# Kernel optimization log

Measured on AMD Instinct MI355X. Metric: run time of the kernel, lower is better.

## Reference

```python
import jax, jax.numpy as jnp
import numpy as np

K = 20  # kNN neighbours (conf.k)

def knn_edge_feats(x, k):
    """x: [B, C, N] -> edge features [B, 2C, N, k] (central || neighbor-central)."""
    xt = jnp.swapaxes(x, 1, 2)                       # [B, N, C]
    sq = jnp.sum(xt * xt, axis=2, keepdims=True)     # [B, N, 1]
    dist = -2.0 * jnp.einsum('bnc,bcm->bnm', xt, x) + sq + jnp.swapaxes(sq, 1, 2)  # [B,N,N]
    idx = jnp.argsort(dist, axis=2)[:, :, 1:k + 1]   # [B, N, k], skip self (col 0)
    nbrs = jax.vmap(lambda xb, ib: xb[:, ib])(x, idx)  # [B, C, N, k]
    central = x[:, :, :, None]                        # [B, C, N, 1]
    return jnp.concatenate([jnp.broadcast_to(central, nbrs.shape), nbrs - central], axis=1)

def edge_conv(x, w, b, k):
    """1x1 conv over edge features, max over k.  x:[B,C,N], w:[Fout,2C], b:[Fout]."""
    ee = knn_edge_feats(x, k)                                   # [B, 2C, N, k]
    y = jnp.einsum('oc,bcnk->bonk', w, ee) + b[None, :, None, None]
    return jnp.max(y, axis=3)                                   # [B, Fout, N]

def setup_inputs() -> dict:
    key = jax.random.key(0)
    ks = iter(jax.random.split(key, 32))
    B, N = 16, 2048
    d = {}
    d['x'] = jax.random.normal(next(ks), (B, 3, N), dtype=jnp.float32)
    def w(shape, scale):
        return jax.random.normal(next(ks), shape, dtype=jnp.float32) * scale
    d['ec0_w'] = w((64, 6), 0.3);    d['ec0_b'] = w((64,), 0.05)
    d['ec1_w'] = w((64, 128), 0.08); d['ec1_b'] = w((64,), 0.05)
    d['ec2_w'] = w((64, 128), 0.08); d['ec2_b'] = w((64,), 0.05)
    d['ec3_w'] = w((128, 128), 0.08); d['ec3_b'] = w((128,), 0.05)
    d['conv0_w'] = w((1024, 320), 0.05); d['conv0_b'] = w((1024,), 0.05)
    d['conv0_s'] = jax.random.uniform(next(ks), (1024,), minval=0.5, maxval=1.5)
    d['conv0_t'] = w((1024,), 0.05)
    d['fc0_w'] = w((512, 1024), 0.03); d['fc0_b'] = w((512,), 0.05)
    d['fc0_s'] = jax.random.uniform(next(ks), (512,), minval=0.5, maxval=1.5)
    d['fc0_t'] = w((512,), 0.05)
    d['fc1_w'] = w((256, 512), 0.04); d['fc1_b'] = w((256,), 0.05)
    d['fc1_s'] = jax.random.uniform(next(ks), (256,), minval=0.5, maxval=1.5)
    d['fc1_t'] = w((256,), 0.05)
    d['fc2_w'] = w((40, 256), 0.06); d['fc2_b'] = w((40,), 0.05)
    d['fc2_s'] = jax.random.uniform(next(ks), (40,), minval=0.5, maxval=1.5)
    d['fc2_t'] = w((40,), 0.05)
    return d

def reference(x, ec0_w, ec0_b, ec1_w, ec1_b, ec2_w, ec2_b, ec3_w, ec3_b,
              conv0_w, conv0_b, conv0_s, conv0_t,
              fc0_w, fc0_b, fc0_s, fc0_t,
              fc1_w, fc1_b, fc1_s, fc1_t,
              fc2_w, fc2_b, fc2_s, fc2_t):
    x1 = edge_conv(x, ec0_w, ec0_b, K)    # [B, 64, N]
    x2 = edge_conv(x1, ec1_w, ec1_b, K)   # [B, 64, N]
    x3 = edge_conv(x2, ec2_w, ec2_b, K)   # [B, 64, N]
    x4 = edge_conv(x3, ec3_w, ec3_b, K)   # [B, 128, N]
    h = jnp.concatenate([x1, x2, x3, x4], axis=1)              # [B, 320, N]
    # conv1dbr: 1x1 conv + BN(affine folded into s,t) + ReLU
    h = jnp.einsum('oc,bcn->bon', conv0_w, h) + conv0_b[None, :, None]
    h = jax.nn.relu(h * conv0_s[None, :, None] + conv0_t[None, :, None])  # [B, 1024, N]
    g = jnp.max(h, axis=2)                                     # [B, 1024]
    # fcbr blocks: linear + BN + ReLU
    g = jax.nn.relu((g @ fc0_w.T + fc0_b) * fc0_s + fc0_t)     # [B, 512]
    g = jax.nn.relu((g @ fc1_w.T + fc1_b) * fc1_s + fc1_t)     # [B, 256]
    g = jax.nn.relu((g @ fc2_w.T + fc2_b) * fc2_s + fc2_t)     # [B, 40]
    return g
```

## Files before the change

kernel.cpp:

```cpp
#include <hip/hip_runtime.h>

#define DEVINL __device__ __forceinline__

static const int NPTS = 2048;

typedef __attribute__((ext_vector_type(8))) short bf16x8;
typedef __attribute__((ext_vector_type(4))) float f32x4;

DEVINL unsigned fenc(float x) {
    int b = __float_as_int(x);
    return (b < 0) ? ~(unsigned)b : ((unsigned)b | 0x80000000u);
}
DEVINL float fdec(unsigned u) {
    return (u & 0x80000000u) ? __int_as_float((int)(u & 0x7fffffffu))
                             : __int_as_float((int)~u);
}
DEVINL unsigned long long u64min(unsigned long long a, unsigned long long b) {
    return (b < a) ? b : a;
}
DEVINL unsigned short f2bf(float x) {
    unsigned u = __float_as_uint(x);
    return (unsigned short)((u + 0x7fffu + ((u >> 16) & 1u)) >> 16);
}
DEVINL float bf2f(unsigned short h) { return __uint_as_float(((unsigned)h) << 16); }

DEVINL void topk20(float v[32], unsigned long long* cand, int lane,
                   int* __restrict__ Iout, int outBase) {
    float t16[16];
#pragma unroll
    for (int i = 0; i < 16; ++i) t16[i] = fminf(v[i], v[i + 16]);
#pragma unroll
    for (int i = 0; i < 8; ++i) t16[i] = fminf(t16[i], t16[i + 8]);
#pragma unroll
    for (int i = 0; i < 4; ++i) t16[i] = fminf(t16[i], t16[i + 4]);
    float s = fminf(fminf(t16[0], t16[1]), fminf(t16[2], t16[3]));
#pragma unroll
    for (int k = 2; k <= 64; k <<= 1) {
#pragma unroll
        for (int j = k >> 1; j >= 1; j >>= 1) {
            float o = __shfl_xor(s, j);
            bool keepmin = (((lane & j) == 0) == ((lane & k) == 0));
            s = keepmin ? fminf(s, o) : fmaxf(s, o);
        }
    }
    const float tau = __shfl(s, 19);
    int cnt = 0;
#pragma unroll
    for (int j = 0; j < 32; ++j) {
        bool pass = (v[j] <= tau);
        unsigned long long mask = __ballot(pass);
        if (pass) {
            int pos = cnt + (int)__popcll(mask & ((1ull << lane) - 1ull));
            if (pos < 64) {
                int col = lane * 4 + (j & 3) + ((j >> 2) << 8);
                cand[pos] = ((unsigned long long)fenc(v[j]) << 32) | (unsigned)col;
            }
        }
        cnt += (int)__popcll(mask);
    }
    if (cnt <= 64) {
        unsigned long long key = (lane < cnt) ? cand[lane] : ~0ull;
#pragma unroll
        for (int k = 2; k <= 64; k <<= 1) {
#pragma unroll
            for (int j = k >> 1; j >= 1; j >>= 1) {
                unsigned long long o = __shfl_xor(key, j);
                bool keepmin = (((lane & j) == 0) == ((lane & k) == 0));
                unsigned long long mn = u64min(key, o);
                unsigned long long mx = (key ^ o) ^ mn;
                key = keepmin ? mn : mx;
            }
        }
        if (lane < 20) Iout[outBase + lane] = (int)(unsigned)(key & 0xffffffffu);
    } else {
        unsigned long long vk[32];
#pragma unroll
        for (int j = 0; j < 32; ++j) {
            int col = lane * 4 + (j & 3) + ((j >> 2) << 8);
            vk[j] = ((unsigned long long)fenc(v[j]) << 32) | (unsigned)col;
        }
        unsigned long long last = 0ull;
        for (int it = 0; it < 20; ++it) {
            unsigned long long q16[16];
#pragma unroll
            for (int i = 0; i < 16; ++i) {
                unsigned long long a = (vk[i] > last) ? vk[i] : ~0ull;
                unsigned long long c = (vk[i + 16] > last) ? vk[i + 16] : ~0ull;
                q16[i] = u64min(a, c);
            }
#pragma unroll
            for (int i = 0; i < 8; ++i) q16[i] = u64min(q16[i], q16[i + 8]);
#pragma unroll
            for (int i = 0; i < 4; ++i) q16[i] = u64min(q16[i], q16[i + 4]);
            unsigned long long best = u64min(u64min(q16[0], q16[1]), u64min(q16[2], q16[3]));
#pragma unroll
            for (int off = 32; off >= 1; off >>= 1) {
                unsigned long long o = __shfl_down(best, off);
                best = u64min(best, o);
            }
            best = __shfl(best, 0);
            if (lane == 0) Iout[outBase + it] = (int)(unsigned)(best & 0xffffffffu);
            last = best;
        }
    }
}

__global__ __launch_bounds__(256) void knnfused_kernel(const float* __restrict__ X, int bs,
                                                       int* __restrict__ Iout) {
    extern __shared__ char smem[];
    float* Dr = (float*)smem;
    float* As = (float*)(smem + 65536);
    unsigned long long* cand = (unsigned long long*)(smem + 67584);
    const int N = NPTS, K = 20;
    const int b = blockIdx.y, n0 = blockIdx.x * 8;
    const float* __restrict__ Xb = X + (size_t)b * bs;
    const int tid = threadIdx.x;
    if (tid < 128) {
        int c = tid >> 1, r4 = (tid & 1) * 4;
        *(float4*)&As[c * 8 + r4] = *(const float4*)&Xb[(size_t)c * N + n0 + r4];
    }
    __syncthreads();
    const int m0 = tid * 4, m1 = 1024 + tid * 4;
    float acc0[8][4], acc1[8][4], sq0[4], sq1[4];
#pragma unroll
    for (int r = 0; r < 8; ++r)
#pragma unroll
        for (int j = 0; j < 4; ++j) { acc0[r][j] = 0.f; acc1[r][j] = 0.f; }
#pragma unroll
    for (int j = 0; j < 4; ++j) { sq0[j] = 0.f; sq1[j] = 0.f; }
#pragma unroll 4
    for (int c = 0; c < 64; ++c) {
        float4 b0 = *(const float4*)&Xb[(size_t)c * N + m0];
        float4 b1 = *(const float4*)&Xb[(size_t)c * N + m1];
        float4 a0 = *(const float4*)&As[c * 8];
        float4 a1 = *(const float4*)&As[c * 8 + 4];
        sq0[0] += b0.x * b0.x; sq0[1] += b0.y * b0.y;
        sq0[2] += b0.z * b0.z; sq0[3] += b0.w * b0.w;
        sq1[0] += b1.x * b1.x; sq1[1] += b1.y * b1.y;
        sq1[2] += b1.z * b1.z; sq1[3] += b1.w * b1.w;
        float av[8] = {a0.x, a0.y, a0.z, a0.w, a1.x, a1.y, a1.z, a1.w};
#pragma unroll
        for (int r = 0; r < 8; ++r) {
            acc0[r][0] += av[r] * b0.x; acc0[r][1] += av[r] * b0.y;
            acc0[r][2] += av[r] * b0.z; acc0[r][3] += av[r] * b0.w;
            acc1[r][0] += av[r] * b1.x; acc1[r][1] += av[r] * b1.y;
            acc1[r][2] += av[r] * b1.z; acc1[r][3] += av[r] * b1.w;
        }
    }
    const float INF = __builtin_inff();
#pragma unroll
    for (int r = 0; r < 8; ++r) {
        const int n = n0 + r;
        float d0[4] = {sq0[0] - 2.f * acc0[r][0], sq0[1] - 2.f * acc0[r][1],
                       sq0[2] - 2.f * acc0[r][2], sq0[3] - 2.f * acc0[r][3]};
        float d1[4] = {sq1[0] - 2.f * acc1[r][0], sq1[1] - 2.f * acc1[r][1],
                       sq1[2] - 2.f * acc1[r][2], sq1[3] - 2.f * acc1[r][3]};
#pragma unroll
        for (int j = 0; j < 4; ++j) {
            if (m0 + j == n) d0[j] = INF;
            if (m1 + j == n) d1[j] = INF;
        }
        *(float4*)&Dr[r * N + m0] = make_float4(d0[0], d0[1], d0[2], d0[3]);
        *(float4*)&Dr[r * N + m1] = make_float4(d1[0], d1[1], d1[2], d1[3]);
    }
    __syncthreads();
    const int w = tid >> 6, lane = tid & 63;
#pragma unroll
    for (int rr = 0; rr < 2; ++rr) {
        const int r = w * 2 + rr;
        const float* __restrict__ rp = &Dr[r * N];
        float v[32];
#pragma unroll
        for (int q = 0; q < 8; ++q) {
            float4 x4 = *(const float4*)&rp[lane * 4 + q * 256];
            v[q * 4 + 0] = x4.x; v[q * 4 + 1] = x4.y;
            v[q * 4 + 2] = x4.z; v[q * 4 + 3] = x4.w;
        }
        topk20(v, cand + w * 64, lane, Iout, (b * N + n0 + r) * K);
    }
}

__global__ __launch_bounds__(256) void select0_kernel(const float* __restrict__ X,
                                                      int* __restrict__ Iout) {
    const int N = NPTS, K = 20;
    __shared__ unsigned long long cand[4][64];
    const int w = threadIdx.x >> 6, lane = threadIdx.x & 63;
    const int rowg = blockIdx.x * 4 + w;
    const int b = rowg >> 11, n = rowg & 2047;
    const float* __restrict__ Xb = X + (size_t)b * 3 * N;
    const float xr = Xb[n], yr = Xb[N + n], zr = Xb[2 * N + n];
    const float INF = __builtin_inff();
    float v[32];
#pragma unroll
    for (int q = 0; q < 8; ++q) {
        const int base = lane * 4 + q * 256;
        const float4 xm = *(const float4*)&Xb[base];
        const float4 ym = *(const float4*)&Xb[N + base];
        const float4 zm = *(const float4*)&Xb[2 * N + base];
        float mx[4] = {xm.x, xm.y, xm.z, xm.w};
        float my[4] = {ym.x, ym.y, ym.z, ym.w};
        float mz[4] = {zm.x, zm.y, zm.z, zm.w};
#pragma unroll
        for (int j = 0; j < 4; ++j) {
            float sq = mx[j] * mx[j] + my[j] * my[j] + mz[j] * mz[j];
            float dot = xr * mx[j] + yr * my[j] + zr * mz[j];
            float d = sq - 2.f * dot;
            v[q * 4 + j] = (base + j == n) ? INF : d;
        }
    }
    topk20(v, &cand[w][0], lane, Iout, (b * N + n) * K);
}

template<int F, int C>
__global__ __launch_bounds__(256) void ut_kernel(const float* __restrict__ X, int bs,
                                                 const float* __restrict__ W,
                                                 const float* __restrict__ bias,
                                                 float* __restrict__ U, float* __restrict__ T) {
    const int N = NPTS;
    __shared__ float Ws2[64][C + 1];
    __shared__ float Wsd[64][C + 1];
    const int n0 = blockIdx.x * 64, f0 = blockIdx.y * 64, b = blockIdx.z;
    const int tid = threadIdx.x;
    for (int i = tid; i < 64 * C; i += 256) {
        int ff = i / C, c = i - ff * C;
        float w1 = W[(f0 + ff) * (2 * C) + c];
        float w2 = W[(f0 + ff) * (2 * C) + C + c];
        Ws2[ff][c] = w2;
        Wsd[ff][c] = w1 - w2;
    }
    __syncthreads();
    const int nt = tid & 15, fg = tid >> 4;
    const float* __restrict__ Xb = X + (size_t)b * bs;
    float au[4][4], av[4][4];
#pragma unroll
    for (int i = 0; i < 4; ++i)
#pragma unroll
        for (int j = 0; j < 4; ++j) { au[i][j] = 0.f; av[i][j] = 0.f; }
#pragma unroll 4
    for (int c = 0; c < C; ++c) {
        const float4 xv = *(const float4*)&Xb[(size_t)c * N + n0 + nt * 4];
#pragma unroll
        for (int fi = 0; fi < 4; ++fi) {
            float w2v = Ws2[fg * 4 + fi][c];
            float wdv = Wsd[fg * 4 + fi][c];
            au[fi][0] += w2v * xv.x; au[fi][1] += w2v * xv.y;
            au[fi][2] += w2v * xv.z; au[fi][3] += w2v * xv.w;
            av[fi][0] += wdv * xv.x; av[fi][1] += wdv * xv.y;
            av[fi][2] += wdv * xv.z; av[fi][3] += wdv * xv.w;
        }
    }
#pragma unroll
    for (int ni = 0; ni < 4; ++ni) {
        int n = n0 + nt * 4 + ni;
        float4 uv = make_float4(au[0][ni], au[1][ni], au[2][ni], au[3][ni]);
        *(float4*)&U[((size_t)b * N + n) * F + f0 + fg * 4] = uv;
    }
#pragma unroll
    for (int fi = 0; fi < 4; ++fi) {
        int f = f0 + fg * 4 + fi;
        float bv = bias[f];
        float4 tv = make_float4(av[fi][0] + bv, av[fi][1] + bv, av[fi][2] + bv, av[fi][3] + bv);
        *(float4*)&T[((size_t)b * F + f) * N + n0 + nt * 4] = tv;
    }
}

template<int F, bool WRITE_F32>
__global__ __launch_bounds__(256) void gathermax_kernel(const float* __restrict__ U,
                                                        const float* __restrict__ T,
                                                        const int* __restrict__ idx,
                                                        float* __restrict__ Y, int bsY,
                                                        unsigned short* __restrict__ HtH,
                                                        unsigned short* __restrict__ HtL,
                                                        int hoff) {
    const int N = NPTS, K = 20, FG = F / 8;
    __shared__ int sidx[32 * 20];
    const int b = blockIdx.y, n0 = blockIdx.x * 32, tid = threadIdx.x;
    const int p = tid >> 3, fg = tid & 7;
    for (int t = tid; t < 32 * K; t += 256) sidx[t] = idx[(b * N + n0) * K + t];
    __syncthreads();
    const int n = n0 + p;
    const float* __restrict__ Ub = U + (size_t)b * N * F;
    const int fbase = fg * FG;
    float mx[FG];
#pragma unroll
    for (int i = 0; i < FG; ++i) mx[i] = -__builtin_inff();
#pragma unroll 4
    for (int j = 0; j < K; ++j) {
        const int r = sidx[p * K + j];
        const float4* up = (const float4*)&Ub[(size_t)r * F + fbase];
#pragma unroll
        for (int q = 0; q < FG / 4; ++q) {
            float4 a = up[q];
            mx[q * 4 + 0] = fmaxf(mx[q * 4 + 0], a.x);
            mx[q * 4 + 1] = fmaxf(mx[q * 4 + 1], a.y);
            mx[q * 4 + 2] = fmaxf(mx[q * 4 + 2], a.z);
            mx[q * 4 + 3] = fmaxf(mx[q * 4 + 3], a.w);
        }
    }
    float val[FG];
#pragma unroll
    for (int i = 0; i < FG; ++i) {
        const int f = fbase + i;
        val[i] = T[((size_t)b * F + f) * N + n] + mx[i];
        if (WRITE_F32) Y[(size_t)b * bsY + (size_t)f * N + n] = val[i];
    }
    unsigned short hs[FG], ls[FG];
#pragma unroll
    for (int i = 0; i < FG; ++i) {
        unsigned short h = f2bf(val[i]);
        hs[i] = h;
        ls[i] = f2bf(val[i] - bf2f(h));
    }
    const size_t hb = ((size_t)b * N + n) * 320 + hoff + fbase;
#pragma unroll
    for (int q = 0; q < FG / 8; ++q) {
        *(int4*)&HtH[hb + q * 8] = *(const int4*)&hs[q * 8];
        *(int4*)&HtL[hb + q * 8] = *(const int4*)&ls[q * 8];
    }
}

__global__ __launch_bounds__(256) void wsplit_kernel(const float* __restrict__ W,
                                                     unsigned short* __restrict__ WH,
                                                     unsigned short* __restrict__ WL) {
    const int e = blockIdx.x * 256 + threadIdx.x;
    float w = W[e];
    unsigned short h = f2bf(w);
    WH[e] = h;
    WL[e] = f2bf(w - bf2f(h));
}

__global__ __launch_bounds__(256) void conv0mfma_kernel(const unsigned short* __restrict__ HtH,
                                                        const unsigned short* __restrict__ HtL,
                                                        const unsigned short* __restrict__ WH,
                                                        const unsigned short* __restrict__ WL,
                                                        unsigned* __restrict__ M) {
    const int N = NPTS;
    __shared__ unsigned short HsH[64][40], HsL[64][40], WsH[128][40], WsL[128][40];
    const int n0 = blockIdx.x * 64, f0 = blockIdx.y * 128, b = blockIdx.z;
    const int tid = threadIdx.x;
    const int wave = tid >> 6, lane = tid & 63;
    const int wm = wave & 1, wf = wave >> 1;
    const int row = lane & 15, quad = lane >> 4;
    f32x4 acc[2][4];
#pragma unroll
    for (int i = 0; i < 2; ++i)
#pragma unroll
        for (int j = 0; j < 4; ++j) acc[i][j] = (f32x4){0.f, 0.f, 0.f, 0.f};

    const int hn = tid >> 2, hq = tid & 3;
    const int wfr = tid >> 1, wq = tid & 1;

    for (int c0 = 0; c0 < 320; c0 += 32) {
        {
            const size_t src = ((size_t)b * N + n0 + hn) * 320 + c0 + hq * 8;
            *(int4*)&HsH[hn][hq * 8] = *(const int4*)&HtH[src];
            *(int4*)&HsL[hn][hq * 8] = *(const int4*)&HtL[src];
        }
        {
            const size_t src = (size_t)(f0 + wfr) * 320 + c0 + wq * 16;
            *(int4*)&WsH[wfr][wq * 16]     = *(const int4*)&WH[src];
            *(int4*)&WsH[wfr][wq * 16 + 8] = *(const int4*)&WH[src + 8];
            *(int4*)&WsL[wfr][wq * 16]     = *(const int4*)&WL[src];
            *(int4*)&WsL[wfr][wq * 16 + 8] = *(const int4*)&WL[src + 8];
        }
        __syncthreads();
        bf16x8 aH[2], aL[2];
#pragma unroll
        for (int mt = 0; mt < 2; ++mt) {
            aH[mt] = *(const bf16x8*)&HsH[wm * 32 + mt * 16 + row][quad * 8];
            aL[mt] = *(const bf16x8*)&HsL[wm * 32 + mt * 16 + row][quad * 8];
        }
#pragma unroll
        for (int nt = 0; nt < 4; ++nt) {
            bf16x8 bH = *(const bf16x8*)&WsH[wf * 64 + nt * 16 + row][quad * 8];
            bf16x8 bL = *(const bf16x8*)&WsL[wf * 64 + nt * 16 + row][quad * 8];
#pragma unroll
            for (int mt = 0; mt < 2; ++mt) {
                acc[mt][nt] = __builtin_amdgcn_mfma_f32_16x16x32_bf16(aH[mt], bH, acc[mt][nt], 0, 0, 0);
                acc[mt][nt] = __builtin_amdgcn_mfma_f32_16x16x32_bf16(aH[mt], bL, acc[mt][nt], 0, 0, 0);
                acc[mt][nt] = __builtin_amdgcn_mfma_f32_16x16x32_bf16(aL[mt], bH, acc[mt][nt], 0, 0, 0);
            }
        }
        __syncthreads();
    }
#pragma unroll
    for (int nt = 0; nt < 4; ++nt) {
        float m = acc[0][nt][0];
#pragma unroll
        for (int r = 1; r < 4; ++r) m = fmaxf(m, acc[0][nt][r]);
#pragma unroll
        for (int r = 0; r < 4; ++r) m = fmaxf(m, acc[1][nt][r]);
        m = fmaxf(m, __shfl_down(m, 16));
        m = fmaxf(m, __shfl_down(m, 32));
        if (quad == 0)
            atomicMax(&M[(b << 10) + f0 + wf * 64 + nt * 16 + row], fenc(m));
    }
}

__global__ __launch_bounds__(256) void fc_kernel(const unsigned* __restrict__ M,
    const float* __restrict__ cb, const float* __restrict__ cs, const float* __restrict__ ct,
    const float* __restrict__ w0, const float* __restrict__ b0, const float* __restrict__ s0, const float* __restrict__ t0,
    const float* __restrict__ w1, const float* __restrict__ b1, const float* __restrict__ s1, const float* __restrict__ t1,
    const float* __restrict__ w2, const float* __restrict__ b2, const float* __restrict__ s2, const float* __restrict__ t2,
    float* __restrict__ out) {
    __shared__ float g0[1024], g1[512], g2[256];
    const int b = blockIdx.x, tid = threadIdx.x;
    for (int f = tid; f < 1024; f += 256) {
        float z = fdec(M[b * 1024 + f]);
        float g = cs[f] * (z + cb[f]) + ct[f];
        g0[f] = fmaxf(g, 0.f);
    }
    __syncthreads();
    for (int f = tid; f < 512; f += 256) {
        const float4* wp = (const float4*)(w0 + (size_t)f * 1024);
        float acc = 0.f;
#pragma unroll 4
        for (int c = 0; c < 256; ++c) {
            float4 wv = wp[c];
            float4 gv = *(const float4*)&g0[c * 4];
            acc += wv.x * gv.x + wv.y * gv.y + wv.z * gv.z + wv.w * gv.w;
        }
        float g = s0[f] * (acc + b0[f]) + t0[f];
        g1[f] = fmaxf(g, 0.f);
    }
    __syncthreads();
    if (tid < 256) {
        const float4* wp = (const float4*)(w1 + (size_t)tid * 512);
        float acc = 0.f;
#pragma unroll 4
        for (int c = 0; c < 128; ++c) {
            float4 wv = wp[c];
            float4 gv = *(const float4*)&g1[c * 4];
            acc += wv.x * gv.x + wv.y * gv.y + wv.z * gv.z + wv.w * gv.w;
        }
        float g = s1[tid] * (acc + b1[tid]) + t1[tid];
        g2[tid] = fmaxf(g, 0.f);
    }
    __syncthreads();
    if (tid < 40) {
        const float4* wp = (const float4*)(w2 + (size_t)tid * 256);
        float acc = 0.f;
#pragma unroll 4
        for (int c = 0; c < 64; ++c) {
            float4 wv = wp[c];
            float4 gv = *(const float4*)&g2[c * 4];
            acc += wv.x * gv.x + wv.y * gv.y + wv.z * gv.z + wv.w * gv.w;
        }
        float g = s2[tid] * (acc + b2[tid]) + t2[tid];
        out[b * 40 + tid] = fmaxf(g, 0.f);
    }
}

extern "C" void kernel_launch(void* const* d_in, const int* in_sizes, int n_in,
                              void* d_out, int out_size, void* d_ws, size_t ws_size,
                              hipStream_t stream) {
    const float* x       = (const float*)d_in[0];
    const float* ec0_w   = (const float*)d_in[1];
    const float* ec0_b   = (const float*)d_in[2];
    const float* ec1_w   = (const float*)d_in[3];
    const float* ec1_b   = (const float*)d_in[4];
    const float* ec2_w   = (const float*)d_in[5];
    const float* ec2_b   = (const float*)d_in[6];
    const float* ec3_w   = (const float*)d_in[7];
    const float* ec3_b   = (const float*)d_in[8];
    const float* conv0_w = (const float*)d_in[9];
    const float* conv0_b = (const float*)d_in[10];
    const float* conv0_s = (const float*)d_in[11];
    const float* conv0_t = (const float*)d_in[12];
    const float* fc0_w   = (const float*)d_in[13];
    const float* fc0_b   = (const float*)d_in[14];
    const float* fc0_s   = (const float*)d_in[15];
    const float* fc0_t   = (const float*)d_in[16];
    const float* fc1_w   = (const float*)d_in[17];
    const float* fc1_b   = (const float*)d_in[18];
    const float* fc1_s   = (const float*)d_in[19];
    const float* fc1_t   = (const float*)d_in[20];
    const float* fc2_w   = (const float*)d_in[21];
    const float* fc2_b   = (const float*)d_in[22];
    const float* fc2_s   = (const float*)d_in[23];
    const float* fc2_t   = (const float*)d_in[24];
    float* out = (float*)d_out;

    char* ws = (char*)d_ws;
    const int B = 16, N = NPTS;
    float* Hc   = (float*)(ws + 0);
    float* U    = (float*)(ws + 41943040);
    float* T    = (float*)(ws + 58720256);
    int*   I    = (int*)  (ws + 75497472);
    unsigned* M = (unsigned*)(ws + 78118912);
    unsigned short* W_hi = (unsigned short*)(ws + 78184448);
    unsigned short* W_lo = (unsigned short*)(ws + 78839808);
    unsigned short* HtH  = (unsigned short*)(ws + 79495168);
    unsigned short* HtL  = (unsigned short*)(ws + 100466688);

    (void)hipFuncSetAttribute((const void*)knnfused_kernel,
                              hipFuncAttributeMaxDynamicSharedMemorySize, 69632);

    dim3 blk(256);
    const int bsX0 = 3 * N, bsH = 320 * N;

    wsplit_kernel<<<dim3(1024 * 320 / 256), blk, 0, stream>>>(conv0_w, W_hi, W_lo);

    select0_kernel<<<dim3(B * N / 4), blk, 0, stream>>>(x, I);
    ut_kernel<64, 3><<<dim3(N / 64, 1, B), blk, 0, stream>>>(x, bsX0, ec0_w, ec0_b, U, T);
    gathermax_kernel<64, true><<<dim3(N / 32, B), blk, 0, stream>>>(U, T, I, Hc, bsH, HtH, HtL, 0);

    const float* Xin[3] = {Hc, Hc + (size_t)64 * N, Hc + (size_t)128 * N};
    const float* ecw[3] = {ec1_w, ec2_w, ec3_w};
    const float* ecb[3] = {ec1_b, ec2_b, ec3_b};
    for (int L = 0; L < 3; ++L) {
        knnfused_kernel<<<dim3(N / 8, B), blk, 69632, stream>>>(Xin[L], bsH, I);
        if (L < 2) {
            ut_kernel<64, 64><<<dim3(N / 64, 1, B), blk, 0, stream>>>(Xin[L], bsH, ecw[L], ecb[L], U, T);
            gathermax_kernel<64, true><<<dim3(N / 32, B), blk, 0, stream>>>(
                U, T, I, Hc + (size_t)(64 * (L + 1)) * N, bsH, HtH, HtL, 64 * (L + 1));
        } else {
            ut_kernel<128, 64><<<dim3(N / 64, 2, B), blk, 0, stream>>>(Xin[L], bsH, ecw[L], ecb[L], U, T);
            gathermax_kernel<128, false><<<dim3(N / 32, B), blk, 0, stream>>>(
                U, T, I, Hc + (size_t)192 * N, bsH, HtH, HtL, 192);
        }
    }

    (void)hipMemsetAsync(M, 0, B * 1024 * sizeof(unsigned), stream);
    conv0mfma_kernel<<<dim3(N / 64, 1024 / 128, B), blk, 0, stream>>>(HtH, HtL, W_hi, W_lo, M);

    fc_kernel<<<dim3(B), blk, 0, stream>>>(M, conv0_b, conv0_s, conv0_t,
                                           fc0_w, fc0_b, fc0_s, fc0_t,
                                           fc1_w, fc1_b, fc1_s, fc1_t,
                                           fc2_w, fc2_b, fc2_s, fc2_t, out);
}
```

Before: 993.0 us.

## Halve kNN distance buffer in LDS by staging rows in two passes

The fused kNN kernel now keeps only 4 distance rows in shared memory (32KB instead of 64KB) and processes the 8 query rows in two halves. The first half's rows are loaded into registers, then the second half is written while top-k runs on the first. The goal is to let more blocks fit per CU (launch bounds now request 4), which raises occupancy for the latency-bound top-k selection. In exchange it adds extra barriers and keeps both accumulator sets and v[32] live at once, which raises register pressure under the tighter launch bound.

```diff
diff --git a/kernel.cpp b/kernel.cpp
--- a/kernel.cpp
+++ b/kernel.cpp
@@ -105,12 +105,11 @@
     }
 }
 
-__global__ __launch_bounds__(256) void knnfused_kernel(const float* __restrict__ X, int bs,
-                                                       int* __restrict__ Iout) {
-    extern __shared__ char smem[];
-    float* Dr = (float*)smem;
-    float* As = (float*)(smem + 65536);
-    unsigned long long* cand = (unsigned long long*)(smem + 67584);
+__global__ __launch_bounds__(256, 4) void knnfused_kernel(const float* __restrict__ X, int bs,
+                                                          int* __restrict__ Iout) {
+    __shared__ float Dr[4 * NPTS];
+    __shared__ float As[64 * 8];
+    __shared__ unsigned long long cand[4 * 64];
     const int N = NPTS, K = 20;
     const int b = blockIdx.y, n0 = blockIdx.x * 8;
     const float* __restrict__ Xb = X + (size_t)b * bs;
@@ -149,7 +148,7 @@
     }
     const float INF = __builtin_inff();
 #pragma unroll
-    for (int r = 0; r < 8; ++r) {
+    for (int r = 0; r < 4; ++r) {
         const int n = n0 + r;
         float d0[4] = {sq0[0] - 2.f * acc0[r][0], sq0[1] - 2.f * acc0[r][1],
                        sq0[2] - 2.f * acc0[r][2], sq0[3] - 2.f * acc0[r][3]};
@@ -165,19 +164,38 @@
     }
     __syncthreads();
     const int w = tid >> 6, lane = tid & 63;
-#pragma unroll
-    for (int rr = 0; rr < 2; ++rr) {
-        const int r = w * 2 + rr;
-        const float* __restrict__ rp = &Dr[r * N];
-        float v[32];
-#pragma unroll
-        for (int q = 0; q < 8; ++q) {
-            float4 x4 = *(const float4*)&rp[lane * 4 + q * 256];
-            v[q * 4 + 0] = x4.x; v[q * 4 + 1] = x4.y;
-            v[q * 4 + 2] = x4.z; v[q * 4 + 3] = x4.w;
-        }
-        topk20(v, cand + w * 64, lane, Iout, (b * N + n0 + r) * K);
-    }
+    float v[32];
+#pragma unroll
+    for (int q = 0; q < 8; ++q) {
+        float4 x4 = *(const float4*)&Dr[w * N + lane * 4 + q * 256];
+        v[q * 4 + 0] = x4.x; v[q * 4 + 1] = x4.y;
+        v[q * 4 + 2] = x4.z; v[q * 4 + 3] = x4.w;
+    }
+    __syncthreads();
+#pragma unroll
+    for (int r = 4; r < 8; ++r) {
+        const int n = n0 + r;
+        float d0[4] = {sq0[0] - 2.f * acc0[r][0], sq0[1] - 2.f * acc0[r][1],
+                       sq0[2] - 2.f * acc0[r][2], sq0[3] - 2.f * acc0[r][3]};
+        float d1[4] = {sq1[0] - 2.f * acc1[r][0], sq1[1] - 2.f * acc1[r][1],
+                       sq1[2] - 2.f * acc1[r][2], sq1[3] - 2.f * acc1[r][3]};
+#pragma unroll
+        for (int j = 0; j < 4; ++j) {
+            if (m0 + j == n) d0[j] = INF;
+            if (m1 + j == n) d1[j] = INF;
+        }
+        *(float4*)&Dr[(r - 4) * N + m0] = make_float4(d0[0], d0[1], d0[2], d0[3]);
+        *(float4*)&Dr[(r - 4) * N + m1] = make_float4(d1[0], d1[1], d1[2], d1[3]);
+    }
+    topk20(v, cand + w * 64, lane, Iout, (b * N + n0 + w) * K);
+    __syncthreads();
+#pragma unroll
+    for (int q = 0; q < 8; ++q) {
+        float4 x4 = *(const float4*)&Dr[w * N + lane * 4 + q * 256];
+        v[q * 4 + 0] = x4.x; v[q * 4 + 1] = x4.y;
+        v[q * 4 + 2] = x4.z; v[q * 4 + 3] = x4.w;
+    }
+    topk20(v, cand + w * 64, lane, Iout, (b * N + n0 + 4 + w) * K);
 }
 
 __global__ __launch_bounds__(256) void select0_kernel(const float* __restrict__ X,
@@ -493,9 +511,6 @@
     unsigned short* HtH  = (unsigned short*)(ws + 79495168);
     unsigned short* HtL  = (unsigned short*)(ws + 100466688);
 
-    (void)hipFuncSetAttribute((const void*)knnfused_kernel,
-                              hipFuncAttributeMaxDynamicSharedMemorySize, 69632);
-
     dim3 blk(256);
     const int bsX0 = 3 * N, bsH = 320 * N;
 
@@ -509,7 +524,7 @@
     const float* ecw[3] = {ec1_w, ec2_w, ec3_w};
     const float* ecb[3] = {ec1_b, ec2_b, ec3_b};
     for (int L = 0; L < 3; ++L) {
-        knnfused_kernel<<<dim3(N / 8, B), blk, 69632, stream>>>(Xin[L], bsH, I);
+        knnfused_kernel<<<dim3(N / 8, B), blk, 0, stream>>>(Xin[L], bsH, I);
         if (L < 2) {
             ut_kernel<64, 64><<<dim3(N / 64, 1, B), blk, 0, stream>>>(Xin[L], bsH, ecw[L], ecb[L], U, T);
             gathermax_kernel<64, true><<<dim3(N / 32, B), blk, 0, stream>>>(
```

After: 1.222 ms. 1.23x slower.
